# Optimization experiments

Hardware: AMD Instinct MI355X
Metric: run time of the kernel (lower is better)

Reference implementation:

```python
import jax, jax.numpy as jnp
import numpy as np

jax.config.update("jax_enable_x64", True)

B = 16384          # batch size (rows of features)
K = 256            # num_unlabel (clusters)
EPS = 0.05         # sinkhorn epsilon
GAMMA = 5.0        # KL regularizer weight
LR = 0.1           # SGD lr for w
MOM = 0.99         # SGD momentum
N_INNER = 3        # sinkhorn iterations
N_OUTER = 10       # outer optimization iterations


def setup_inputs() -> dict:
    key = jax.random.key(0)
    features = jax.random.normal(key, (B, K), dtype=jnp.float32)
    w = jnp.ones((1, K), dtype=jnp.float32) / K  # torch Parameter init: ones/K
    return {"features": features, "w": w, "head": 0}


def _sinkhorn(logits, w):
    """SinkhornKnopp_im.forward: logits [B,K] -> Q [B,K] (float64), preds=logits64."""
    logits64 = logits.astype(jnp.float64)
    Q = jnp.exp(logits64 / EPS).T            # [K, B]
    Q = Q / jnp.sum(Q)
    K2 = jax.nn.softmax(w, axis=1).astype(jnp.float64)  # [1, K] marginal prior
    Bn = Q.shape[1]
    for _ in range(N_INNER):
        Q = Q / jnp.sum(Q, axis=1, keepdims=True)       # row normalize
        Q = Q * K2.T                                    # scale rows by prior
        Q = Q / jnp.sum(Q, axis=0, keepdims=True)       # column normalize
        Q = Q / Bn
    Q = Q * Bn
    return Q.T, logits64                                # [B, K], [B, K]


def _total_loss(w, features):
    Q, preds = _sinkhorn(features, w)
    loss = -jnp.mean(jnp.sum(Q * preds, axis=1))
    # KLDivLoss(batchmean): input = log_softmax(w).T [K,1], target = softmax(w0).T = 1/K
    logw = jax.nn.log_softmax(w, axis=1)[0]             # [K]
    t = jnp.float32(1.0 / K)
    reg = jnp.sum(t * (jnp.log(t) - logw)) / K
    return loss + GAMMA * reg.astype(jnp.float64), Q


def reference(features, w, head):
    features = jax.lax.stop_gradient(features)  # features.detach()

    def step(carry, _):
        w, buf, _ = carry
        (_, Q), g = jax.value_and_grad(_total_loss, has_aux=True)(w, features)
        # clip_grad_norm_(params, 1)
        norm = jnp.sqrt(jnp.sum(g.astype(jnp.float64) ** 2)).astype(g.dtype)
        g = g * jnp.minimum(jnp.float32(1.0), jnp.float32(1.0) / (norm + 1e-6))
        # SGD with momentum 0.99 (buf starts at 0 -> first buf = g, matching torch)
        buf = MOM * buf + g
        w = w - LR * buf
        return (w, buf, Q), None

    Q0 = jnp.zeros((features.shape[0], K), dtype=jnp.float64)
    (w_f, buf_f, Q), _ = jax.lax.scan(
        step, (w, jnp.zeros_like(w), Q0), None, length=N_OUTER
    )
    return Q  # Q from the last outer iteration (computed with pre-update w)
```

## Files before the change

kernel.cpp:

```cpp
#include <hip/hip_runtime.h>


namespace {

constexpr int KDIM = 256;
constexpr int NBLK = 256;
constexpr int ROWS = 64;
constexpr int NRED = 16;
constexpr float L2E20 = 28.853900817779268f;

constexpr size_t P_DBL   = 2ull * 256 * 512;
constexpr size_t FIN_OFF = P_DBL;
constexpr size_t FIN_PAR = 6ull * 16 * 256 * 2;
constexpr size_t FIN_DBL = 2 * FIN_PAR;
constexpr size_t FLAG_OFF_DBL = FIN_OFF + FIN_DBL;
constexpr int FLAG_U32 = 256 * 32;

__device__ __forceinline__ double fast_exp_d(double x) {
  const double LOG2E  = 1.4426950408889634074;
  const double LN2_HI = 6.93147180369123816490e-01;
  const double LN2_LO = 1.90821492927058770002e-10;
  double n = rint(x * LOG2E);
  double t = fma(-n, LN2_HI, x);
  t = fma(-n, LN2_LO, t);
  double p = 2.4801587301587302e-05;
  p = fma(p, t, 1.9841269841269841e-04);
  p = fma(p, t, 1.3888888888888889e-03);
  p = fma(p, t, 8.3333333333333333e-03);
  p = fma(p, t, 4.1666666666666664e-02);
  p = fma(p, t, 1.6666666666666666e-01);
  p = fma(p, t, 0.5);
  p = fma(p, t, 1.0);
  p = fma(p, t, 1.0);
  long long ni = (long long)n;
  double s = __longlong_as_double((unsigned long long)(ni + 1023LL) << 52);
  return p * s;
}

__device__ __forceinline__ double wave_sum_d(double v) {
#pragma unroll
  for (int o = 32; o > 0; o >>= 1) v += __shfl_down(v, o);
  return v;
}
__device__ __forceinline__ double wave_max_d(double v) {
#pragma unroll
  for (int o = 32; o > 0; o >>= 1) v = fmax(v, __shfl_down(v, o));
  return v;
}

__device__ __forceinline__ double pload(const double* p) {
  return __hip_atomic_load(p, __ATOMIC_RELAXED, __HIP_MEMORY_SCOPE_AGENT);
}
__device__ __forceinline__ void pstore(double* p, double v) {
  __hip_atomic_store(p, v, __ATOMIC_RELAXED, __HIP_MEMORY_SCOPE_AGENT);
}

}

__global__ __launch_bounds__(256) void kInitWS(double* __restrict__ ws) {
  const double QN = __builtin_nan("");
  size_t gid = (size_t)blockIdx.x * 256 + threadIdx.x;
  size_t stride = (size_t)gridDim.x * 256;
  double* fin = ws + FIN_OFF;
  for (size_t j = gid; j < FIN_DBL; j += stride) fin[j] = QN;
  unsigned* fl = (unsigned*)(ws + FLAG_OFF_DBL);
  if (gid < FLAG_U32) fl[gid] = 0u;
}

__global__ __launch_bounds__(256, 1) void sink_main(
    const float* __restrict__ feat, const float* __restrict__ w_in,
    float* __restrict__ out, double* __restrict__ ws) {
  __shared__ float  Et[ROWS * KDIM];
  __shared__ float  Ft[ROWS * KDIM];
  __shared__ double alpha[KDIM];
  __shared__ double tmp1[KDIM];
  __shared__ double tmp2[KDIM];
  __shared__ double sfin[32];
  __shared__ double v1s[ROWS], v2s[ROWS], v3s[ROWS];
  __shared__ double grow[ROWS], wrow[ROWS], sbr[ROWS];
  __shared__ float  mrow[ROWS];
  __shared__ double sred[8];

  const int t = threadIdx.x, bid = blockIdx.x;
  const int wv = t >> 6, lane = t & 63;
  const int b0 = bid * ROWS;
  const double QN = __builtin_nan("");

  double* P = ws;
  double* fin = ws + FIN_OFF;
  unsigned* flag1 = (unsigned*)(ws + FLAG_OFF_DBL);

  auto blk_sum = [&](double v) -> double {
    v = wave_sum_d(v);
    __syncthreads();
    if (lane == 0) sred[wv] = v;
    __syncthreads();
    return sred[0] + sred[1] + sred[2] + sred[3];
  };
  auto blk_max = [&](double v) -> double {
    v = wave_max_d(v);
    __syncthreads();
    if (lane == 0) sred[wv + 4] = v;
    __syncthreads();
    return fmax(fmax(sred[4], sred[5]), fmax(sred[6], sred[7]));
  };

  auto allreduce = [&](unsigned ph, int kind, bool pair, int par,
                       double pa, double pb, double& r1, double& r2) {
    double* row = P + (((size_t)(ph & 1)) * 256 + bid) * 512;
    pstore(&row[2 * t], pa);
    if (pair) pstore(&row[2 * t + 1], pb);
    __syncthreads();
    if (t == 0)
      __hip_atomic_store(&flag1[bid * 32], ph, __ATOMIC_RELAXED,
                         __HIP_MEMORY_SCOPE_AGENT);
    if (bid < NRED) {
      const int rep = t >> 4, c = t & 15;
      {
        double* dst = fin + (size_t)(1 - par) * FIN_PAR +
                      (size_t)kind * 8192 + (size_t)rep * 512 +
                      2 * (size_t)(bid * 16 + c);
        pstore(dst, QN);
        pstore(dst + 1, QN);
      }
      {
        const unsigned* f = &flag1[t * 32];
        while (__hip_atomic_load(f, __ATOMIC_RELAXED,
                                 __HIP_MEMORY_SCOPE_AGENT) < ph)
          __builtin_amdgcn_s_sleep(1);
      }
      __syncthreads();
      const double* base = P + ((size_t)(ph & 1)) * 131072;
      const int k = bid * 16 + c;
      double a1 = 0.0, a2 = 0.0;
#pragma unroll
      for (int i = 0; i < 16; ++i) {
        const double* rr = base + (size_t)(rep + 16 * i) * 512;
        a1 += pload(&rr[2 * k]);
        if (pair) a2 += pload(&rr[2 * k + 1]);
      }
      tmp1[t] = a1;
      if (pair) tmp2[t] = a2;
      __syncthreads();
      if (t < 16) {
        double s = 0.0;
#pragma unroll
        for (int g2 = 0; g2 < 16; ++g2) s += tmp1[g2 * 16 + t];
        sfin[2 * t] = s;
        if (!pair) sfin[2 * t + 1] = 0.0;
      } else if (pair && t < 32) {
        int c2 = t - 16;
        double s = 0.0;
#pragma unroll
        for (int g2 = 0; g2 < 16; ++g2) s += tmp2[g2 * 16 + c2];
        sfin[2 * c2 + 1] = s;
      }
      __syncthreads();
      {
        double* dst = fin + (size_t)par * FIN_PAR + (size_t)kind * 8192 +
                      (size_t)rep * 512 + 2 * (size_t)(bid * 16 + c);
        pstore(dst, sfin[2 * c]);
        if (pair) pstore(dst + 1, sfin[2 * c + 1]);
      }
    }
    {
      const double* e = fin + (size_t)par * FIN_PAR + (size_t)kind * 8192 +
                        (size_t)(bid & 15) * 512 + 2 * (size_t)t;
      double a;
      for (;;) {
        a = pload(e);
        if (!__builtin_isnan(a)) break;
        __builtin_amdgcn_s_sleep(1);
      }
      r1 = a;
      if (pair) {
        double b;
        for (;;) {
          b = pload(e + 1);
          if (!__builtin_isnan(b)) break;
          __builtin_amdgcn_s_sleep(1);
        }
        r2 = b;
      }
    }
    __syncthreads();
  };

  auto row_pass = [&](double* dstv) {
    double a0 = alpha[4 * lane + 0], a1 = alpha[4 * lane + 1];
    double a2 = alpha[4 * lane + 2], a3 = alpha[4 * lane + 3];
#pragma unroll 4
    for (int r = wv; r < ROWS; r += 4) {
      float4 e4 = ((const float4*)(Et + r * KDIM))[lane];
      double s1 = a0 * (double)e4.x + a1 * (double)e4.y +
                  a2 * (double)e4.z + a3 * (double)e4.w;
      s1 = wave_sum_d(s1);
      if (lane == 0) dstv[r] = s1;
    }
  };
  auto col_partial = [&]() -> double {
    double a = 0.0;
#pragma unroll 8
    for (int r = 0; r < ROWS; ++r) a += (double)Et[r * KDIM + t] * wrow[r];
    return a;
  };

  {
    const float4* src = (const float4*)(feat + (size_t)b0 * KDIM);
    float4* dst = (float4*)Ft;
#pragma unroll
    for (int s = 0; s < 16; ++s) dst[s * 256 + t] = src[s * 256 + t];
  }
  __syncthreads();
  for (int r = wv; r < ROWS; r += 4) {
    float4 f4 = ((const float4*)(Ft + r * KDIM))[lane];
    float m = fmaxf(fmaxf(f4.x, f4.y), fmaxf(f4.z, f4.w));
#pragma unroll
    for (int o = 32; o > 0; o >>= 1) m = fmaxf(m, __shfl_down(m, o));
    if (lane == 0) {
      mrow[r] = m;
      sbr[r] = fast_exp_d(20.0 * (double)m);
    }
  }
  __syncthreads();
  double pu0 = 0.0;
#pragma unroll 8
  for (int r = 0; r < ROWS; ++r) {
    float e = exp2f((Ft[r * KDIM + t] - mrow[r]) * L2E20);
    Et[r * KDIM + t] = e;
    pu0 += (double)e * sbr[r];
  }
  float w_t = w_in[t], buf_t = 0.0f;
  double k2_t;
  {
    double x = (double)w_t;
    double m = blk_max(x);
    double e = fast_exp_d(x - m);
    double s = blk_sum(e);
    k2_t = e / s;
  }
  unsigned ph = 1;
  double u0_t, dmy;
  allreduce(ph, 0, false, 0, pu0, 0.0, u0_t, dmy);

  for (int it = 0; it < 10; ++it) {
    const int p = it & 1;
    double u1_t, u2_t;

    alpha[t] = k2_t / u0_t;
    __syncthreads();
    row_pass(v1s);
    __syncthreads();
    if (t < ROWS) wrow[t] = 1.0 / (16384.0 * v1s[t]);
    __syncthreads();
    {
      double pa = col_partial();
      ++ph; allreduce(ph, 1, false, p, pa, 0.0, u1_t, dmy);
    }

    alpha[t] = k2_t / u1_t;
    __syncthreads();
    row_pass(v2s);
    __syncthreads();
    if (t < ROWS) wrow[t] = 1.0 / (16384.0 * v2s[t]);
    __syncthreads();
    {
      double pa = col_partial();
      ++ph; allreduce(ph, 2, false, p, pa, 0.0, u2_t, dmy);
    }

    if (it == 9) {
      alpha[t] = k2_t / u2_t;
      __syncthreads();
      row_pass(v3s);
      __syncthreads();
      if (t < ROWS) wrow[t] = 1.0 / v3s[t];
      __syncthreads();
      double a3 = alpha[t];
#pragma unroll 4
      for (int r = 0; r < ROWS; ++r)
        out[(size_t)(b0 + r) * KDIM + t] =
            (float)(a3 * (double)Et[r * KDIM + t] * wrow[r]);
      return;
    }

    alpha[t] = k2_t / u2_t;
    __syncthreads();
    {
      double a0 = alpha[4 * lane + 0], a1 = alpha[4 * lane + 1];
      double a2 = alpha[4 * lane + 2], a3 = alpha[4 * lane + 3];
#pragma unroll 2
      for (int r = wv; r < ROWS; r += 4) {
        float4 e4 = ((const float4*)(Et + r * KDIM))[lane];
        float4 f4 = ((const float4*)(Ft + r * KDIM))[lane];
        double p0 = a0 * (double)e4.x, p1 = a1 * (double)e4.y;
        double p2 = a2 * (double)e4.z, p3 = a3 * (double)e4.w;
        double s1 = p0 + p1 + p2 + p3;
        double s2 = p0 * (double)f4.x + p1 * (double)f4.y +
                    p2 * (double)f4.z + p3 * (double)f4.w;
        s1 = wave_sum_d(s1);
        s2 = wave_sum_d(s2);
        if (lane == 0) {
          v3s[r] = s1;
          grow[r] = s2 / (16384.0 * s1 * s1);
        }
      }
    }
    __syncthreads();
    if (t < ROWS) wrow[t] = -1.0 / (16384.0 * v3s[t]);
    __syncthreads();
    double gd_t, t3_t;
    {
      double ac1 = 0.0, ac2 = 0.0;
#pragma unroll 8
      for (int r = 0; r < ROWS; ++r) {
        double ed = (double)Et[r * KDIM + t];
        ac1 += ed * (double)Ft[r * KDIM + t] * wrow[r];
        ac2 += ed * grow[r];
      }
      ++ph; allreduce(ph, 3, true, p, ac1, ac2, gd_t, t3_t);
    }

    alpha[t] = -(gd_t + t3_t) * k2_t / (u2_t * u2_t);
    __syncthreads();
    row_pass(grow);
    __syncthreads();
    if (t < ROWS) wrow[t] = -grow[t] / (16384.0 * v2s[t] * v2s[t]);
    __syncthreads();
    double ga2_t;
    {
      double pa = col_partial();
      ++ph; allreduce(ph, 4, false, p, pa, 0.0, ga2_t, dmy);
    }

    alpha[t] = -ga2_t * k2_t / (u1_t * u1_t);
    __syncthreads();
    row_pass(grow);
    __syncthreads();
    if (t < ROWS) wrow[t] = -grow[t] / (16384.0 * v1s[t] * v1s[t]);
    __syncthreads();
    double ga1_t;
    {
      double pa = col_partial();
      ++ph; allreduce(ph, 5, false, p, pa, 0.0, ga1_t, dmy);
    }

    {
      double gk2 = (gd_t + t3_t) / u2_t + ga2_t / u1_t + ga1_t / u0_t;
      double dot = blk_sum(k2_t * gk2);
      double gw = k2_t * (gk2 - dot) + 5.0 * (k2_t / 256.0 - 1.0 / 65536.0);
      double n2 = blk_sum(gw * gw);
      float normf = (float)sqrt(n2);
      float sc = fminf(1.0f, 1.0f / (normf + 1e-6f));
      float g = (float)gw * sc;
      buf_t = 0.99f * buf_t + g;
      w_t = w_t - 0.1f * buf_t;
      double x = (double)w_t;
      double m = blk_max(x);
      double e = fast_exp_d(x - m);
      double s = blk_sum(e);
      k2_t = e / s;
    }
  }
}

extern "C" void kernel_launch(void* const* d_in, const int* in_sizes, int n_in,
                              void* d_out, int out_size, void* d_ws,
                              size_t ws_size, hipStream_t stream) {
  (void)in_sizes; (void)n_in; (void)out_size; (void)ws_size;
  const float* feat = (const float*)d_in[0];
  const float* w_in = (const float*)d_in[1];
  float* out = (float*)d_out;
  double* ws = (double*)d_ws;

  kInitWS<<<128, 256, 0, stream>>>(ws);
  sink_main<<<NBLK, 256, 0, stream>>>(feat, w_in, out, ws);
}
```

Baseline: 559.4 us.

## Replace two-stage flag/NaN allreduce with per-phase global atomic accumulators

The cross-block allreduce no longer writes partials that 16 reducer blocks gather and republish through NaN-sentinel buffers. Each thread now atomically adds its partial into a per-phase global slot, and each block bumps a per-phase arrival counter and spins until all 256 blocks have arrived, then reads the sum back. This removes a second polling round and the reducer-block bottleneck, at the cost of 256-way contended float64 atomics per slot and sums whose order is no longer deterministic. Every phase gets its own zero-initialized slot, so no buffers are reused across phases.

```diff
diff --git a/kernel.cpp b/kernel.cpp
--- a/kernel.cpp
+++ b/kernel.cpp
@@ -6,15 +6,14 @@
 constexpr int KDIM = 256;
 constexpr int NBLK = 256;
 constexpr int ROWS = 64;
-constexpr int NRED = 16;
 constexpr float L2E20 = 28.853900817779268f;
 
-constexpr size_t P_DBL   = 2ull * 256 * 512;
-constexpr size_t FIN_OFF = P_DBL;
-constexpr size_t FIN_PAR = 6ull * 16 * 256 * 2;
-constexpr size_t FIN_DBL = 2 * FIN_PAR;
-constexpr size_t FLAG_OFF_DBL = FIN_OFF + FIN_DBL;
-constexpr int FLAG_U32 = 256 * 32;
+constexpr int NPH = 64;
+constexpr int SLOT_DBL = 8;
+constexpr size_t ACC_DBL = (size_t)NPH * KDIM * SLOT_DBL;
+constexpr size_t CNT_OFF_DBL = ACC_DBL;
+constexpr int CNT_STRIDE = 16;
+constexpr int CNT_U32 = NPH * CNT_STRIDE;
 
 __device__ __forceinline__ double fast_exp_d(double x) {
   const double LOG2E  = 1.4426950408889634074;
@@ -51,20 +50,15 @@
 __device__ __forceinline__ double pload(const double* p) {
   return __hip_atomic_load(p, __ATOMIC_RELAXED, __HIP_MEMORY_SCOPE_AGENT);
 }
-__device__ __forceinline__ void pstore(double* p, double v) {
-  __hip_atomic_store(p, v, __ATOMIC_RELAXED, __HIP_MEMORY_SCOPE_AGENT);
-}
 
 }
 
 __global__ __launch_bounds__(256) void kInitWS(double* __restrict__ ws) {
-  const double QN = __builtin_nan("");
   size_t gid = (size_t)blockIdx.x * 256 + threadIdx.x;
   size_t stride = (size_t)gridDim.x * 256;
-  double* fin = ws + FIN_OFF;
-  for (size_t j = gid; j < FIN_DBL; j += stride) fin[j] = QN;
-  unsigned* fl = (unsigned*)(ws + FLAG_OFF_DBL);
-  if (gid < FLAG_U32) fl[gid] = 0u;
+  for (size_t j = gid; j < ACC_DBL; j += stride) ws[j] = 0.0;
+  unsigned* c = (unsigned*)(ws + CNT_OFF_DBL);
+  for (size_t j = gid; j < (size_t)CNT_U32; j += stride) c[j] = 0u;
 }
 
 __global__ __launch_bounds__(256, 1) void sink_main(
@@ -73,9 +67,6 @@
   __shared__ float  Et[ROWS * KDIM];
   __shared__ float  Ft[ROWS * KDIM];
   __shared__ double alpha[KDIM];
-  __shared__ double tmp1[KDIM];
-  __shared__ double tmp2[KDIM];
-  __shared__ double sfin[32];
   __shared__ double v1s[ROWS], v2s[ROWS], v3s[ROWS];
   __shared__ double grow[ROWS], wrow[ROWS], sbr[ROWS];
   __shared__ float  mrow[ROWS];
@@ -84,11 +75,9 @@
   const int t = threadIdx.x, bid = blockIdx.x;
   const int wv = t >> 6, lane = t & 63;
   const int b0 = bid * ROWS;
-  const double QN = __builtin_nan("");
-
-  double* P = ws;
-  double* fin = ws + FIN_OFF;
-  unsigned* flag1 = (unsigned*)(ws + FLAG_OFF_DBL);
+
+  double* acc = ws;
+  unsigned* cnt = (unsigned*)(ws + CNT_OFF_DBL);
 
   auto blk_sum = [&](double v) -> double {
     v = wave_sum_d(v);
@@ -105,85 +94,26 @@
     return fmax(fmax(sred[4], sred[5]), fmax(sred[6], sred[7]));
   };
 
-  auto allreduce = [&](unsigned ph, int kind, bool pair, int par,
-                       double pa, double pb, double& r1, double& r2) {
-    double* row = P + (((size_t)(ph & 1)) * 256 + bid) * 512;
-    pstore(&row[2 * t], pa);
-    if (pair) pstore(&row[2 * t + 1], pb);
-    __syncthreads();
-    if (t == 0)
-      __hip_atomic_store(&flag1[bid * 32], ph, __ATOMIC_RELAXED,
-                         __HIP_MEMORY_SCOPE_AGENT);
-    if (bid < NRED) {
-      const int rep = t >> 4, c = t & 15;
-      {
-        double* dst = fin + (size_t)(1 - par) * FIN_PAR +
-                      (size_t)kind * 8192 + (size_t)rep * 512 +
-                      2 * (size_t)(bid * 16 + c);
-        pstore(dst, QN);
-        pstore(dst + 1, QN);
+  auto allreduce = [&](unsigned ph, bool pair, double pa, double pb,
+                       double& r1, double& r2) {
+    double* slot = acc + ((size_t)ph * KDIM + t) * SLOT_DBL;
+    unsafeAtomicAdd(slot, pa);
+    if (pair) unsafeAtomicAdd(slot + 1, pb);
+    asm volatile("s_waitcnt vmcnt(0)" ::: "memory");
+    __syncthreads();
+    if (t == 0) {
+      unsigned* c = cnt + (size_t)ph * CNT_STRIDE;
+      unsigned prev = __hip_atomic_fetch_add(c, 1u, __ATOMIC_RELAXED,
+                                             __HIP_MEMORY_SCOPE_AGENT);
+      if (prev != NBLK - 1) {
+        while (__hip_atomic_load(c, __ATOMIC_RELAXED,
+                                 __HIP_MEMORY_SCOPE_AGENT) < NBLK)
+          __builtin_amdgcn_s_sleep(2);
       }
-      {
-        const unsigned* f = &flag1[t * 32];
-        while (__hip_atomic_load(f, __ATOMIC_RELAXED,
-                                 __HIP_MEMORY_SCOPE_AGENT) < ph)
-          __builtin_amdgcn_s_sleep(1);
-      }
-      __syncthreads();
-      const double* base = P + ((size_t)(ph & 1)) * 131072;
-      const int k = bid * 16 + c;
-      double a1 = 0.0, a2 = 0.0;
-#pragma unroll
-      for (int i = 0; i < 16; ++i) {
-        const double* rr = base + (size_t)(rep + 16 * i) * 512;
-        a1 += pload(&rr[2 * k]);
-        if (pair) a2 += pload(&rr[2 * k + 1]);
-      }
-      tmp1[t] = a1;
-      if (pair) tmp2[t] = a2;
-      __syncthreads();
-      if (t < 16) {
-        double s = 0.0;
-#pragma unroll
-        for (int g2 = 0; g2 < 16; ++g2) s += tmp1[g2 * 16 + t];
-        sfin[2 * t] = s;
-        if (!pair) sfin[2 * t + 1] = 0.0;
-      } else if (pair && t < 32) {
-        int c2 = t - 16;
-        double s = 0.0;
-#pragma unroll
-        for (int g2 = 0; g2 < 16; ++g2) s += tmp2[g2 * 16 + c2];
-        sfin[2 * c2 + 1] = s;
-      }
-      __syncthreads();
-      {
-        double* dst = fin + (size_t)par * FIN_PAR + (size_t)kind * 8192 +
-                      (size_t)rep * 512 + 2 * (size_t)(bid * 16 + c);
-        pstore(dst, sfin[2 * c]);
-        if (pair) pstore(dst + 1, sfin[2 * c + 1]);
-      }
-    }
-    {
-      const double* e = fin + (size_t)par * FIN_PAR + (size_t)kind * 8192 +
-                        (size_t)(bid & 15) * 512 + 2 * (size_t)t;
-      double a;
-      for (;;) {
-        a = pload(e);
-        if (!__builtin_isnan(a)) break;
-        __builtin_amdgcn_s_sleep(1);
-      }
-      r1 = a;
-      if (pair) {
-        double b;
-        for (;;) {
-          b = pload(e + 1);
-          if (!__builtin_isnan(b)) break;
-          __builtin_amdgcn_s_sleep(1);
-        }
-        r2 = b;
-      }
-    }
-    __syncthreads();
+    }
+    __syncthreads();
+    r1 = pload(slot);
+    if (pair) r2 = pload(slot + 1);
   };
 
   auto row_pass = [&](double* dstv) {
@@ -239,12 +169,11 @@
     double s = blk_sum(e);
     k2_t = e / s;
   }
-  unsigned ph = 1;
+  unsigned ph = 0;
   double u0_t, dmy;
-  allreduce(ph, 0, false, 0, pu0, 0.0, u0_t, dmy);
+  allreduce(ph, false, pu0, 0.0, u0_t, dmy);
 
   for (int it = 0; it < 10; ++it) {
-    const int p = it & 1;
     double u1_t, u2_t;
 
     alpha[t] = k2_t / u0_t;
@@ -255,7 +184,7 @@
     __syncthreads();
     {
       double pa = col_partial();
-      ++ph; allreduce(ph, 1, false, p, pa, 0.0, u1_t, dmy);
+      ++ph; allreduce(ph, false, pa, 0.0, u1_t, dmy);
     }
 
     alpha[t] = k2_t / u1_t;
@@ -266,7 +195,7 @@
     __syncthreads();
     {
       double pa = col_partial();
-      ++ph; allreduce(ph, 2, false, p, pa, 0.0, u2_t, dmy);
+      ++ph; allreduce(ph, false, pa, 0.0, u2_t, dmy);
     }
 
     if (it == 9) {
@@ -318,7 +247,7 @@
         ac1 += ed * (double)Ft[r * KDIM + t] * wrow[r];
         ac2 += ed * grow[r];
       }
-      ++ph; allreduce(ph, 3, true, p, ac1, ac2, gd_t, t3_t);
+      ++ph; allreduce(ph, true, ac1, ac2, gd_t, t3_t);
     }
 
     alpha[t] = -(gd_t + t3_t) * k2_t / (u2_t * u2_t);
@@ -330,7 +259,7 @@
     double ga2_t;
     {
       double pa = col_partial();
-      ++ph; allreduce(ph, 4, false, p, pa, 0.0, ga2_t, dmy);
+      ++ph; allreduce(ph, false, pa, 0.0, ga2_t, dmy);
     }
 
     alpha[t] = -ga2_t * k2_t / (u1_t * u1_t);
@@ -342,7 +271,7 @@
     double ga1_t;
     {
       double pa = col_partial();
-      ++ph; allreduce(ph, 5, false, p, pa, 0.0, ga1_t, dmy);
+      ++ph; allreduce(ph, false, pa, 0.0, ga1_t, dmy);
     }
 
     {
```

Result: slower. 1.018 ms (+81.9%).
